# Optimization experiments

Measured on AMD Instinct MI355X. Metric: run time of the kernel, lower is better.

## Reference

```python
import jax, jax.numpy as jnp
import numpy as np

B, N, D = 1, 4096, 512
H, HD = 8, 64
NBINS = 512
CAND = 64
SCALE = 1.0 / np.sqrt(HD)
MAX_NORM = 1.0 - 1e-5
TWO_PI = 2.0 * np.pi


def _project(x):
    # Poincare-ball style projection: clip L2 norm of each point to MAX_NORM.
    n = jnp.sqrt(jnp.sum(x * x, axis=-1, keepdims=True))
    s = jnp.minimum(1.0, MAX_NORM / jnp.maximum(n, 1e-12))
    return x * s


def _bins(x):
    # Deterministic geometric binning (DavisCache stand-in): quantize the
    # angle of the first two coordinates into NBINS bins.
    ang = jnp.arctan2(x[..., 1], x[..., 0])  # (-pi, pi]
    b = jnp.floor((ang / TWO_PI + 0.5) * NBINS)
    return jnp.clip(b, 0, NBINS - 1).astype(jnp.int32)


def setup_inputs() -> dict:
    key0 = jax.random.key(0)
    ks = jax.random.split(key0, 12)
    w = 0.02  # typical init scale for projection weights
    return {
        "query": jax.random.normal(ks[0], (B, N, D), dtype=jnp.float32),
        "key": jax.random.normal(ks[1], (B, N, D), dtype=jnp.float32),
        "value": jax.random.normal(ks[2], (B, N, D), dtype=jnp.float32),
        "Wq": jax.random.normal(ks[3], (D, D), dtype=jnp.float32) * w,
        "bq": jnp.zeros((D,), dtype=jnp.float32),
        "Wk": jax.random.normal(ks[4], (D, D), dtype=jnp.float32) * w,
        "bk": jnp.zeros((D,), dtype=jnp.float32),
        "Wv": jax.random.normal(ks[5], (D, D), dtype=jnp.float32) * w,
        "bv": jnp.zeros((D,), dtype=jnp.float32),
        "Wo": jax.random.normal(ks[6], (D, D), dtype=jnp.float32) * w,
        "bo": jnp.zeros((D,), dtype=jnp.float32),
    }


def reference(query, key, value, Wq, bq, Wk, bk, Wv, bv, Wo, bo):
    Bq, Nq, Dm = query.shape
    Nk = key.shape[1]
    # projections + split heads -> (B, H, N, HD)
    q = (query @ Wq.T + bq).reshape(Bq, Nq, H, HD).transpose(0, 2, 1, 3)
    k = (key @ Wk.T + bk).reshape(Bq, Nk, H, HD).transpose(0, 2, 1, 3)
    v = (value @ Wv.T + bv).reshape(Bq, Nk, H, HD).transpose(0, 2, 1, 3)
    q = _project(q)
    k = _project(k)

    # geometric binning; candidate keys for a query are those whose bin is
    # within radius 1 of the query's bin (neighboring_bins, radius=1).
    qb = _bins(q)  # (B, H, Nq) int32
    kb = _bins(k)  # (B, H, Nk) int32
    mask = jnp.abs(qb[..., :, None] - kb[..., None, :]) <= 1  # (B,H,Nq,Nk)
    # fallback: if a query has no candidates, attend over all keys
    any_valid = jnp.any(mask, axis=-1, keepdims=True)
    eff = jnp.where(any_valid, mask, True)
    # keep only the first CAND candidates per query (by key index)
    rank = jnp.cumsum(eff.astype(jnp.int32), axis=-1) - 1
    sel = eff & (rank < CAND)

    scores = jnp.einsum("bhqd,bhkd->bhqk", q, k) * SCALE
    scores = jnp.where(sel, scores, -jnp.inf)
    attn = jax.nn.softmax(scores, axis=-1)  # dropout p=0.0 (eval mode)
    out = jnp.einsum("bhqk,bhkd->bhqd", attn, v)

    out = out.transpose(0, 2, 1, 3).reshape(Bq, Nq, Dm)
    return out @ Wo.T + bo
```

## Files before the change

kernel.cpp:

```cpp
#include <hip/hip_runtime.h>
#include <math.h>

typedef unsigned short u16;
typedef __attribute__((ext_vector_type(8))) short v8bf;
typedef __attribute__((ext_vector_type(4))) float f32x4;

#define N_TOK 4096
#define DMODEL 512
#define NHEAD 8
#define HDIM 64
#define CANDN 64
#define NBINS 512
#define BINCAP 64
#define QCAP 128
#define ATT_SCALE 0.125f
#define MAX_NORM_F 0.99999f

__device__ __forceinline__ u16 f2bf(float f) {
  union { float f; unsigned int i; } v; v.f = f;
  unsigned int x = v.i;
  return (u16)((x + 0x7fffu + ((x >> 16) & 1u)) >> 16);
}
__device__ __forceinline__ uint4 pack8v(const float4 x0, const float4 x1) {
  union { u16 h[8]; uint4 u; } r;
  r.h[0] = f2bf(x0.x); r.h[1] = f2bf(x0.y); r.h[2] = f2bf(x0.z); r.h[3] = f2bf(x0.w);
  r.h[4] = f2bf(x1.x); r.h[5] = f2bf(x1.y); r.h[6] = f2bf(x1.z); r.h[7] = f2bf(x1.w);
  return r.u;
}

__global__ __launch_bounds__(256) void bins_kernel(
    const float* __restrict__ query, const float* __restrict__ key_,
    const float* __restrict__ Wq, const float* __restrict__ Wk,
    int* __restrict__ qb, int* __restrict__ kb,
    unsigned char* __restrict__ flags, int* __restrict__ khist)
{
  __shared__ float xs[16 * 516];
  const int blk = blockIdx.x;
  const int tid = threadIdx.x;

  if (blk >= 512) {
    int4 z4; z4.x = 0; z4.y = 0; z4.z = 0; z4.w = 0;
#pragma unroll
    for (int i = 0; i < 8; ++i) ((int4*)khist)[tid + i * 256] = z4;
    return;
  }

  const int isk  = blk >> 8;
  const int tile = blk & 255;
  const float* X = isk ? key_ : query;
  const float* W = isk ? Wk : Wq;

#pragma unroll
  for (int i = 0; i < 8; ++i) {
    const int flat = i * 1024 + tid * 4;
    const int row = flat >> 9, col = flat & 511;
    *(float4*)&xs[row * 516 + col] = *(const float4*)(X + (tile * 16 + row) * DMODEL + col);
  }
  __syncthreads();

  const int n_local = tid >> 4;
  const int pair = tid & 15;
  const int h = pair >> 1, coord = pair & 1;
  const float* wrow = W + ((h << 6) + coord) * DMODEL;
  const float* xrow = &xs[n_local * 516];

  double c0 = 0.0, c1 = 0.0, c2 = 0.0, c3 = 0.0;
  for (int k = 0; k < DMODEL; k += 4) {
    const float4 xv = *(const float4*)(xrow + k);
    const float4 wv = *(const float4*)(wrow + k);
    c0 = fma((double)xv.x, (double)wv.x, c0);
    c1 = fma((double)xv.y, (double)wv.y, c1);
    c2 = fma((double)xv.z, (double)wv.z, c2);
    c3 = fma((double)xv.w, (double)wv.w, c3);
  }
  const double a = (c0 + c1) + (c2 + c3);
  const double other = __shfl_xor(a, 1);
  if (coord == 0) {
    const double a0 = a, a1 = other;
    const int n = tile * 16 + n_local;
    double ang = atan2(a1, a0);
    double t = (ang / 6.283185307179586 + 0.5) * 512.0;
    int b = (int)floor(t);
    b = b < 0 ? 0 : (b > 511 ? 511 : b);
    (isk ? kb : qb)[(h << 12) + n] = b;

    const double r = sqrt(a0 * a0 + a1 * a1);
    const double dist = fabs(t - nearbyint(t));
    const double margin = fmin(0.45, 3.3e-4 / fmax(r, 1e-30) + 5e-5);
    flags[(isk << 15) | (h << 12) | n] = (dist < margin) ? 1 : 0;
  }
}

__device__ float fdlibm_atanf(float x) {
#pragma clang fp contract(off)
  const float atanhi[4] = {4.6364760399e-01f, 7.8539812565e-01f,
                           9.8279368877e-01f, 1.5707962513e+00f};
  const float atanlo[4] = {5.0121582440e-09f, 3.7748947079e-08f,
                           3.4473217170e-08f, 7.5497894159e-08f};
  const float aT[5] = {3.3333328366e-01f, -1.9999158382e-01f, 1.4253635705e-01f,
                       -1.0648017377e-01f, 6.1687607318e-02f};
  unsigned ix = __float_as_uint(x);
  const unsigned sign = ix >> 31;
  ix &= 0x7fffffffu;
  int id;
  float z, w, s1, s2;
  if (ix >= 0x4c800000u) {
    z = atanhi[3] + 0x1p-120f;
    return sign ? -z : z;
  }
  if (ix < 0x3ee00000u) {
    if (ix < 0x39800000u) return x;
    id = -1;
  } else {
    x = fabsf(x);
    if (ix < 0x3f980000u) {
      if (ix < 0x3f300000u) { id = 0; x = (2.0f * x - 1.0f) / (2.0f + x); }
      else                  { id = 1; x = (x - 1.0f) / (x + 1.0f); }
    } else {
      if (ix < 0x401c0000u) { id = 2; x = (x - 1.5f) / (1.0f + 1.5f * x); }
      else                  { id = 3; x = -1.0f / x; }
    }
  }
  z = x * x;
  w = z * z;
  s1 = z * (aT[0] + w * (aT[2] + w * aT[4]));
  s2 = w * (aT[1] + w * aT[3]);
  if (id < 0) return x - x * (s1 + s2);
  z = atanhi[id] - ((x * (s1 + s2) - atanlo[id]) - x);
  return sign ? -z : z;
}

__device__ float fdlibm_atan2f(float y, float x) {
#pragma clang fp contract(off)
  const float pi = 3.1415927410e+00f, pi_lo = -8.7422776573e-08f;
  const unsigned hx = __float_as_uint(x), hy = __float_as_uint(y);
  if (hx == 0x3f800000u) return fdlibm_atanf(y);
  const unsigned m = ((hy >> 31) & 1u) | ((hx >> 30) & 2u);
  const unsigned ix = hx & 0x7fffffffu, iy = hy & 0x7fffffffu;
  if (iy == 0u) {
    switch (m) { case 0: case 1: return y; case 2: return pi; default: return -pi; }
  }
  if (ix == 0u) return (m & 1u) ? -1.57079637050628662f : 1.57079637050628662f;
  float z;
  if (ix + (26u << 23) < iy) {
    z = 1.57079637050628662f;
    return (m & 1u) ? -z : z;
  }
  if ((m & 2u) && iy + (26u << 23) < ix) z = 0.0f;
  else z = fdlibm_atanf(fabsf(y / x));
  switch (m) {
    case 0: return z;
    case 1: return -z;
    case 2: return pi - (z - pi_lo);
    default: return (z - pi_lo) - pi;
  }
}

__global__ __launch_bounds__(256) void fixgemm_kernel(
    const float* __restrict__ query, const float* __restrict__ key_,
    const float* __restrict__ value,
    const float* __restrict__ Wq, const float* __restrict__ Wk,
    const float* __restrict__ Wv,
    const float* __restrict__ bq, const float* __restrict__ bk,
    const float* __restrict__ bv,
    const unsigned char* __restrict__ flags,
    int* __restrict__ qb, int* __restrict__ kb,
    u16* __restrict__ Qb, u16* __restrict__ Kb, u16* __restrict__ Vb)
{
  __shared__ __align__(16) char smem[30720];
  __shared__ int wle[64];
  __shared__ int wlc;

  const int blk = blockIdx.x;
  const int tid = threadIdx.x;

  if (blk < 512) {
    const int slice = blk;
    if (tid == 0) wlc = 0;
    __syncthreads();
    if (tid < 128) {
      const int flat = (slice << 7) + tid;
      if (flags[flat]) {
        const int p = atomicAdd(&wlc, 1);
        if (p < 64) wle[p] = flat;
      }
    }
    __syncthreads();
    int nw = wlc; if (nw > 64) nw = 64;
    const int w = tid >> 6, d = tid & 63;
    for (int e = w; e < nw; e += 4) {
      const int flat = wle[e];
      const int n = flat & 4095;
      const int h = (flat >> 12) & 7;
      const int isk = flat >> 15;
      const float* xr = (isk ? key_ : query) + n * DMODEL;
      const float* wr = (isk ? Wk : Wq) + ((h << 6) + d) * DMODEL;
      float acc = 0.0f;
      for (int k = 0; k < DMODEL; k += 16) {
        const float4 xa = *(const float4*)(xr + k);
        const float4 xb = *(const float4*)(xr + k + 4);
        const float4 xc = *(const float4*)(xr + k + 8);
        const float4 xd = *(const float4*)(xr + k + 12);
        const float4 wa = *(const float4*)(wr + k);
        const float4 wb = *(const float4*)(wr + k + 4);
        const float4 wc = *(const float4*)(wr + k + 8);
        const float4 wd = *(const float4*)(wr + k + 12);
        acc = __fmaf_rn(xa.x, wa.x, acc); acc = __fmaf_rn(xa.y, wa.y, acc);
        acc = __fmaf_rn(xa.z, wa.z, acc); acc = __fmaf_rn(xa.w, wa.w, acc);
        acc = __fmaf_rn(xb.x, wb.x, acc); acc = __fmaf_rn(xb.y, wb.y, acc);
        acc = __fmaf_rn(xb.z, wb.z, acc); acc = __fmaf_rn(xb.w, wb.w, acc);
        acc = __fmaf_rn(xc.x, wc.x, acc); acc = __fmaf_rn(xc.y, wc.y, acc);
        acc = __fmaf_rn(xc.z, wc.z, acc); acc = __fmaf_rn(xc.w, wc.w, acc);
        acc = __fmaf_rn(xd.x, wd.x, acc); acc = __fmaf_rn(xd.y, wd.y, acc);
        acc = __fmaf_rn(xd.z, wd.z, acc); acc = __fmaf_rn(xd.w, wd.w, acc);
      }
      {
#pragma clang fp contract(off)
        const float sq = acc * acc;
        float rr[8];
#pragma unroll
        for (int j = 0; j < 8; ++j) rr[j] = __shfl(sq, j);
        for (int i = 8; i < 64; i += 8) {
#pragma unroll
          for (int j = 0; j < 8; ++j) rr[j] += __shfl(sq, i + j);
        }
        const float ss = ((rr[0] + rr[1]) + (rr[2] + rr[3])) +
                         ((rr[4] + rr[5]) + (rr[6] + rr[7]));
        const float nrm = __fsqrt_rn(ss);
        const float s = fminf(1.0f, 0.99999f / fmaxf(nrm, 1e-12f));
        const float c0 = __shfl(acc, 0) * s;
        const float c1 = __shfl(acc, 1) * s;
        const float cr = (float)atan2((double)c1, (double)c0);
        const float fd = fdlibm_atan2f(c1, c0);
        const float tol = fmaxf(fabsf(cr) * 6e-7f, 1e-30f);
        const float ang = (fabsf(fd - cr) <= tol) ? fd : cr;
        const float t = ((ang / 6.2831854820251465f) + 0.5f) * 512.0f;
        int b = (int)floorf(t);
        b = b < 0 ? 0 : (b > 511 ? 511 : b);
        if (d == 0) (isk ? kb : qb)[(h << 12) + n] = b;
      }
    }
    return;
  }

  u16* As = (u16*)smem;
  u16* Ws = (u16*)(smem + 10240);

  const int rel = blk - 512;
  const int z = rel >> 8;
  const int rem = rel & 255;
  const int bm = (rem & 63) * 64;
  const int bn = (rem >> 6) * 128;

  const float* X  = (z == 0) ? query : (z == 1) ? key_ : value;
  const float* WF = (z == 0) ? Wq : (z == 1) ? Wk : Wv;
  const float* bias = (z == 0) ? bq : (z == 1) ? bk : bv;
  u16* O          = (z == 0) ? Qb : (z == 1) ? Kb : Vb;

  const int lane = tid & 63;
  const int wave = tid >> 6;
  const int ra  = tid >> 2;
  const int oa  = (tid & 3) * 8;
  const int wm = (wave & 1) * 32;
  const int wn = (wave >> 1) * 64;
  const int l15 = lane & 15;
  const int quad = lane >> 4;

  f32x4 acc[2][4] = {};

  float4 a0f0 = *(const float4*)(X + (bm + ra) * DMODEL + oa);
  float4 a0f1 = *(const float4*)(X + (bm + ra) * DMODEL + oa + 4);
  float4 w0f0 = *(const float4*)(WF + (bn + ra) * DMODEL + oa);
  float4 w0f1 = *(const float4*)(WF + (bn + ra) * DMODEL + oa + 4);
  float4 w1f0 = *(const float4*)(WF + (bn + ra + 64) * DMODEL + oa);
  float4 w1f1 = *(const float4*)(WF + (bn + ra + 64) * DMODEL + oa + 4);

  for (int kt = 0; kt < DMODEL; kt += 32) {
    const int p = (kt >> 5) & 1;
    *(uint4*)&As[p * 2560 + ra * 40 + oa] = pack8v(a0f0, a0f1);
    *(uint4*)&Ws[p * 5120 + ra * 40 + oa] = pack8v(w0f0, w0f1);
    *(uint4*)&Ws[p * 5120 + (ra + 64) * 40 + oa] = pack8v(w1f0, w1f1);
    __syncthreads();
    if (kt + 32 < DMODEL) {
      a0f0 = *(const float4*)(X + (bm + ra) * DMODEL + kt + 32 + oa);
      a0f1 = *(const float4*)(X + (bm + ra) * DMODEL + kt + 32 + oa + 4);
      w0f0 = *(const float4*)(WF + (bn + ra) * DMODEL + kt + 32 + oa);
      w0f1 = *(const float4*)(WF + (bn + ra) * DMODEL + kt + 32 + oa + 4);
      w1f0 = *(const float4*)(WF + (bn + ra + 64) * DMODEL + kt + 32 + oa);
      w1f1 = *(const float4*)(WF + (bn + ra + 64) * DMODEL + kt + 32 + oa + 4);
    }
    v8bf af[2], bfr[4];
#pragma unroll
    for (int i = 0; i < 2; ++i)
      af[i] = *(const v8bf*)&As[p * 2560 + (wm + i * 16 + l15) * 40 + quad * 8];
#pragma unroll
    for (int j = 0; j < 4; ++j)
      bfr[j] = *(const v8bf*)&Ws[p * 5120 + (wn + j * 16 + l15) * 40 + quad * 8];
#pragma unroll
    for (int i = 0; i < 2; ++i)
#pragma unroll
      for (int j = 0; j < 4; ++j)
        acc[i][j] = __builtin_amdgcn_mfma_f32_16x16x32_bf16(af[i], bfr[j], acc[i][j], 0, 0, 0);
  }

  float bval[4];
#pragma unroll
  for (int j = 0; j < 4; ++j) bval[j] = bias[bn + wn + j * 16 + l15];
  const int h = (bn + wn) >> 6;

#pragma unroll
  for (int i = 0; i < 2; ++i) {
#pragma unroll
    for (int r = 0; r < 4; ++r) {
      const int row = bm + wm + i * 16 + quad * 4 + r;
      float v0 = acc[i][0][r] + bval[0];
      float v1 = acc[i][1][r] + bval[1];
      float v2 = acc[i][2][r] + bval[2];
      float v3 = acc[i][3][r] + bval[3];
      if (z != 2) {
        float ss = v0 * v0 + v1 * v1 + v2 * v2 + v3 * v3;
#pragma unroll
        for (int o = 1; o < 16; o <<= 1) ss += __shfl_xor(ss, o);
        const float s = fminf(1.0f, MAX_NORM_F / fmaxf(sqrtf(ss), 1e-12f));
        v0 *= s; v1 *= s; v2 *= s; v3 *= s;
      }
      const int base = (((h << 12) + row) << 6) + l15;
      O[base +  0] = f2bf(v0); O[base + 16] = f2bf(v1);
      O[base + 32] = f2bf(v2); O[base + 48] = f2bf(v3);
    }
  }
}

__global__ __launch_bounds__(256) void bin_hist_kernel(
    const int* __restrict__ kb, const int* __restrict__ qb,
    int* __restrict__ khist, u16* __restrict__ blist,
    int* __restrict__ qhist, u16* __restrict__ qlist)
{
  const int h = blockIdx.x;
  const int type = blockIdx.y;
  const int* src = type ? qb : kb;
  int* hist = type ? qhist : khist;
  u16* list = type ? qlist : blist;
  const int cap = type ? QCAP : BINCAP;

  const int i = blockIdx.z * 256 + threadIdx.x;
  const int b = src[(h << 12) + i];
  const int pos = atomicAdd(&hist[(h << 9) + b], 1);
  if (pos < cap) list[((h << 9) + b) * cap + pos] = (u16)i;
}

__global__ __launch_bounds__(64) void attn_bin_kernel(
    const u16* __restrict__ Qb, const u16* __restrict__ Kb,
    const u16* __restrict__ Vb, const int* __restrict__ qhist,
    const u16* __restrict__ qlist, const int* __restrict__ khist,
    const u16* __restrict__ blist, u16* __restrict__ aout)
{
  __shared__ u16 kf[4 * 2 * 4 * 16 * 8];
  __shared__ u16 pf[16 * 72];
  __shared__ u16 s_cand[64];
  __shared__ int s_qg[16];

  const int hb = blockIdx.x;
  const int h = hb >> 9;
  const int b = hb & 511;
  int qcnt = qhist[hb];
  if (qcnt > QCAP) qcnt = QCAP;
  if (qcnt == 0) return;

  const int lane = threadIdx.x;
  const int l15 = lane & 15;
  const int quad = lane >> 4;

  int v0 = 0xFFFF, v1 = 0xFFFF, v2 = 0xFFFF;
  int c0 = 0, c1 = 0, c2 = 0;
  if (b > 0) {
    c0 = khist[(h << 9) + b - 1];
    if (c0 > BINCAP) c0 = BINCAP;
    if (lane < c0) v0 = (int)blist[(((h << 9) + b - 1) << 6) + lane];
  }
  {
    c1 = khist[(h << 9) + b];
    if (c1 > BINCAP) c1 = BINCAP;
    if (lane < c1) v1 = (int)blist[(((h << 9) + b) << 6) + lane];
  }
  if (b < NBINS - 1) {
    c2 = khist[(h << 9) + b + 1];
    if (c2 > BINCAP) c2 = BINCAP;
    if (lane < c2) v2 = (int)blist[(((h << 9) + b + 1) << 6) + lane];
  }

  int r0 = 0, r1 = 0, r2 = 0;
#pragma unroll 8
  for (int j = 0; j < 64; ++j) {
    const int w0 = __shfl(v0, j);
    const int w1 = __shfl(v1, j);
    const int w2 = __shfl(v2, j);
    r0 += (w0 < v0) + (w1 < v0) + (w2 < v0);
    r1 += (w0 < v1) + (w1 < v1) + (w2 < v1);
    r2 += (w0 < v2) + (w1 < v2) + (w2 < v2);
  }
  const int tot = c0 + c1 + c2;
  const int ccnt = tot < CANDN ? tot : CANDN;
  const int ccnt_eff = (tot == 0) ? 64 : ccnt;
  if (tot == 0) {
    s_cand[lane] = (u16)lane;
  } else {
    if (v0 != 0xFFFF && r0 < CANDN) s_cand[r0] = (u16)v0;
    if (v1 != 0xFFFF && r1 < CANDN) s_cand[r1] = (u16)v1;
    if (v2 != 0xFFFF && r2 < CANDN) s_cand[r2] = (u16)v2;
  }
  __syncthreads();
  if (tot > 0 && lane >= ccnt) s_cand[lane] = s_cand[0];
  __syncthreads();

  {
    const int r = lane >> 3, s = lane & 7;
    const int ks = s >> 2, qd = s & 3;
#pragma unroll
    for (int it = 0; it < 8; ++it) {
      const int key = it * 8 + r;
      const int c = s_cand[key];
      const uint4 kv = *(const uint4*)(Kb + ((h << 18) | (c << 6)) + s * 8);
      const int idx = ((((key >> 4) * 2 + ks) * 4 + qd) * 16 + (key & 15)) * 8;
      *(uint4*)&kf[idx] = kv;
    }
  }
  __syncthreads();
  v8bf akf[4][2];
#pragma unroll
  for (int t = 0; t < 4; ++t)
#pragma unroll
    for (int ks = 0; ks < 2; ++ks)
      akf[t][ks] = *(const v8bf*)&kf[(((t * 2 + ks) * 4 + quad) * 16 + l15) * 8];
  __syncthreads();

  {
    const int r = lane >> 3, s = lane & 7;
    const int nt = s >> 1, d0 = (s & 1) * 8;
#pragma unroll
    for (int it = 0; it < 8; ++it) {
      const int key = it * 8 + r;
      const int c = s_cand[key];
      union { u16 hh[8]; uint4 u; } vv;
      vv.u = *(const uint4*)(Vb + ((h << 18) | (c << 6)) + s * 8);
      const int kstep = key >> 5, qd = (key >> 3) & 3, j = key & 7;
#pragma unroll
      for (int m = 0; m < 8; ++m)
        kf[(((nt * 2 + kstep) * 4 + qd) * 16 + d0 + m) * 8 + j] = vv.hh[m];
    }
  }
  __syncthreads();
  v8bf bvf[4][2];
#pragma unroll
  for (int t = 0; t < 4; ++t)
#pragma unroll
    for (int ks = 0; ks < 2; ++ks)
      bvf[t][ks] = *(const v8bf*)&kf[(((t * 2 + ks) * 4 + quad) * 16 + l15) * 8];

  const int nchunk = (qcnt + 15) >> 4;
  for (int ci = 0; ci < nchunk; ++ci) {
    const int base = ci << 4;
    const int qcn = min(16, qcnt - base);
    __syncthreads();
    if (lane < 16) {
      int idx = base + lane;
      if (idx > qcnt - 1) idx = qcnt - 1;
      s_qg[lane] = (int)qlist[(hb << 7) + idx];
    }
    __syncthreads();

    const u16* qrow = Qb + ((h << 18) | (s_qg[l15] << 6));
    v8bf bq[2];
#pragma unroll
    for (int ks = 0; ks < 2; ++ks)
      bq[ks] = *(const v8bf*)(qrow + ks * 32 + quad * 8);

    float sc[16];
    __builtin_amdgcn_s_setprio(1);
#pragma unroll
    for (int t = 0; t < 4; ++t) {
      f32x4 sa = {0.f, 0.f, 0.f, 0.f};
      sa = __builtin_amdgcn_mfma_f32_16x16x32_bf16(akf[t][0], bq[0], sa, 0, 0, 0);
      sa = __builtin_amdgcn_mfma_f32_16x16x32_bf16(akf[t][1], bq[1], sa, 0, 0, 0);
#pragma unroll
      for (int r = 0; r < 4; ++r) {
        const int key = t * 16 + quad * 4 + r;
        sc[t * 4 + r] = (key < ccnt_eff) ? sa[r] * ATT_SCALE : -INFINITY;
      }
    }
    __builtin_amdgcn_s_setprio(0);
    float mx = sc[0];
#pragma unroll
    for (int i = 1; i < 16; ++i) mx = fmaxf(mx, sc[i]);
    mx = fmaxf(mx, __shfl_xor(mx, 16));
    mx = fmaxf(mx, __shfl_xor(mx, 32));
    float sum = 0.0f;
    float pe[16];
#pragma unroll
    for (int i = 0; i < 16; ++i) { pe[i] = __expf(sc[i] - mx); sum += pe[i]; }
    sum += __shfl_xor(sum, 16);
    sum += __shfl_xor(sum, 32);
    const float inv = 1.0f / sum;

    __syncthreads();
#pragma unroll
    for (int t = 0; t < 4; ++t)
#pragma unroll
      for (int r = 0; r < 4; ++r)
        pf[l15 * 72 + t * 16 + quad * 4 + r] = f2bf(pe[t * 4 + r] * inv);
    __syncthreads();

    v8bf ap[2];
#pragma unroll
    for (int ks = 0; ks < 2; ++ks)
      ap[ks] = *(const v8bf*)&pf[l15 * 72 + ks * 32 + quad * 8];

    __builtin_amdgcn_s_setprio(1);
#pragma unroll
    for (int nt = 0; nt < 4; ++nt) {
      f32x4 o = {0.f, 0.f, 0.f, 0.f};
      o = __builtin_amdgcn_mfma_f32_16x16x32_bf16(ap[0], bvf[nt][0], o, 0, 0, 0);
      o = __builtin_amdgcn_mfma_f32_16x16x32_bf16(ap[1], bvf[nt][1], o, 0, 0, 0);
#pragma unroll
      for (int r = 0; r < 4; ++r) {
        const int row = quad * 4 + r;
        if (row < qcn)
          aout[s_qg[row] * DMODEL + (h << 6) + nt * 16 + l15] = f2bf(o[r]);
      }
    }
    __builtin_amdgcn_s_setprio(0);
  }
}

__global__ __launch_bounds__(256) void gemm_out_kernel(
    const u16* __restrict__ A, const float* __restrict__ WF,
    const float* __restrict__ bias, float* __restrict__ O)
{
  __shared__ u16 As[2][64 * 40];
  __shared__ u16 Ws[2][64 * 40];

  const int tid  = threadIdx.x;
  const int lane = tid & 63;
  const int wave = tid >> 6;
  const int ra  = tid >> 2;
  const int oa  = (tid & 3) * 8;

  const int bm = blockIdx.x * 64;
  const int bn = blockIdx.y * 64;
  const int wm = (wave & 1) * 32;
  const int wn = (wave >> 1) * 32;
  const int l15 = lane & 15;
  const int quad = lane >> 4;

  f32x4 acc[2][2] = {};

  uint4 a0 = *(const uint4*)(A + (bm + ra) * DMODEL + oa);
  float4 w0f0 = *(const float4*)(WF + (bn + ra) * DMODEL + oa);
  float4 w0f1 = *(const float4*)(WF + (bn + ra) * DMODEL + oa + 4);

  for (int kt = 0; kt < DMODEL; kt += 32) {
    const int p = (kt >> 5) & 1;
    *(uint4*)&As[p][ra * 40 + oa] = a0;
    *(uint4*)&Ws[p][ra * 40 + oa] = pack8v(w0f0, w0f1);
    __syncthreads();
    if (kt + 32 < DMODEL) {
      a0 = *(const uint4*)(A + (bm + ra) * DMODEL + kt + 32 + oa);
      w0f0 = *(const float4*)(WF + (bn + ra) * DMODEL + kt + 32 + oa);
      w0f1 = *(const float4*)(WF + (bn + ra) * DMODEL + kt + 32 + oa + 4);
    }
    v8bf af[2], bfr[2];
#pragma unroll
    for (int i = 0; i < 2; ++i)
      af[i] = *(const v8bf*)&As[p][(wm + i * 16 + l15) * 40 + quad * 8];
#pragma unroll
    for (int j = 0; j < 2; ++j)
      bfr[j] = *(const v8bf*)&Ws[p][(wn + j * 16 + l15) * 40 + quad * 8];
#pragma unroll
    for (int i = 0; i < 2; ++i)
#pragma unroll
      for (int j = 0; j < 2; ++j)
        acc[i][j] = __builtin_amdgcn_mfma_f32_16x16x32_bf16(af[i], bfr[j], acc[i][j], 0, 0, 0);
  }

#pragma unroll
  for (int j = 0; j < 2; ++j) {
    const int cg = bn + wn + j * 16 + l15;
    const float bval = bias[cg];
#pragma unroll
    for (int i = 0; i < 2; ++i) {
      const int rbase = bm + wm + i * 16 + quad * 4;
#pragma unroll
      for (int r = 0; r < 4; ++r)
        O[(rbase + r) * DMODEL + cg] = acc[i][j][r] + bval;
    }
  }
}

extern "C" void kernel_launch(void* const* d_in, const int* in_sizes, int n_in,
                              void* d_out, int out_size, void* d_ws, size_t ws_size,
                              hipStream_t stream) {
  const float* query = (const float*)d_in[0];
  const float* key_  = (const float*)d_in[1];
  const float* value = (const float*)d_in[2];
  const float* Wq = (const float*)d_in[3];
  const float* bq = (const float*)d_in[4];
  const float* Wk = (const float*)d_in[5];
  const float* bk = (const float*)d_in[6];
  const float* Wv = (const float*)d_in[7];
  const float* bv = (const float*)d_in[8];
  const float* Wo = (const float*)d_in[9];
  const float* bo = (const float*)d_in[10];

  char* ws = (char*)d_ws;
  u16* Qb    = (u16*)(ws + 14680064);
  u16* Kb    = (u16*)(ws + 18874368);
  u16* Vb    = (u16*)(ws + 23068672);
  u16* aout  = (u16*)(ws + 27262976);
  int* qb    = (int*)(ws + 31457280);
  int* kb    = (int*)(ws + 31588352);
  unsigned char* flags = (unsigned char*)(ws + 31719424);
  int* khist = (int*)(ws + 31784960);
  int* qhist = (int*)(ws + 31801344);
  u16* blist = (u16*)(ws + 31817728);
  u16* qlist = (u16*)(ws + 32342016);

  bins_kernel<<<513, 256, 0, stream>>>(
      query, key_, Wq, Wk, qb, kb, flags, khist);
  fixgemm_kernel<<<1280, 256, 0, stream>>>(
      query, key_, value, Wq, Wk, Wv, bq, bk, bv,
      flags, qb, kb, Qb, Kb, Vb);
  bin_hist_kernel<<<dim3(8, 2, 16), 256, 0, stream>>>(
      kb, qb, khist, blist, qhist, qlist);
  attn_bin_kernel<<<4096, 64, 0, stream>>>(
      Qb, Kb, Vb, qhist, qlist, khist, blist, aout);
  gemm_out_kernel<<<dim3(64, 8), 256, 0, stream>>>(aout, Wo, bo, (float*)d_out);
}
```

Before: 194.9 us.

## Fuse bin fix-up into bins kernel and histogram into projection GEMM

After: 194.8 us. Within noise of the previous version (-0.1%).

```diff
diff --git a/kernel.cpp b/kernel.cpp
--- a/kernel.cpp
+++ b/kernel.cpp
@@ -26,69 +26,6 @@
   r.h[0] = f2bf(x0.x); r.h[1] = f2bf(x0.y); r.h[2] = f2bf(x0.z); r.h[3] = f2bf(x0.w);
   r.h[4] = f2bf(x1.x); r.h[5] = f2bf(x1.y); r.h[6] = f2bf(x1.z); r.h[7] = f2bf(x1.w);
   return r.u;
-}
-
-__global__ __launch_bounds__(256) void bins_kernel(
-    const float* __restrict__ query, const float* __restrict__ key_,
-    const float* __restrict__ Wq, const float* __restrict__ Wk,
-    int* __restrict__ qb, int* __restrict__ kb,
-    unsigned char* __restrict__ flags, int* __restrict__ khist)
-{
-  __shared__ float xs[16 * 516];
-  const int blk = blockIdx.x;
-  const int tid = threadIdx.x;
-
-  if (blk >= 512) {
-    int4 z4; z4.x = 0; z4.y = 0; z4.z = 0; z4.w = 0;
-#pragma unroll
-    for (int i = 0; i < 8; ++i) ((int4*)khist)[tid + i * 256] = z4;
-    return;
-  }
-
-  const int isk  = blk >> 8;
-  const int tile = blk & 255;
-  const float* X = isk ? key_ : query;
-  const float* W = isk ? Wk : Wq;
-
-#pragma unroll
-  for (int i = 0; i < 8; ++i) {
-    const int flat = i * 1024 + tid * 4;
-    const int row = flat >> 9, col = flat & 511;
-    *(float4*)&xs[row * 516 + col] = *(const float4*)(X + (tile * 16 + row) * DMODEL + col);
-  }
-  __syncthreads();
-
-  const int n_local = tid >> 4;
-  const int pair = tid & 15;
-  const int h = pair >> 1, coord = pair & 1;
-  const float* wrow = W + ((h << 6) + coord) * DMODEL;
-  const float* xrow = &xs[n_local * 516];
-
-  double c0 = 0.0, c1 = 0.0, c2 = 0.0, c3 = 0.0;
-  for (int k = 0; k < DMODEL; k += 4) {
-    const float4 xv = *(const float4*)(xrow + k);
-    const float4 wv = *(const float4*)(wrow + k);
-    c0 = fma((double)xv.x, (double)wv.x, c0);
-    c1 = fma((double)xv.y, (double)wv.y, c1);
-    c2 = fma((double)xv.z, (double)wv.z, c2);
-    c3 = fma((double)xv.w, (double)wv.w, c3);
-  }
-  const double a = (c0 + c1) + (c2 + c3);
-  const double other = __shfl_xor(a, 1);
-  if (coord == 0) {
-    const double a0 = a, a1 = other;
-    const int n = tile * 16 + n_local;
-    double ang = atan2(a1, a0);
-    double t = (ang / 6.283185307179586 + 0.5) * 512.0;
-    int b = (int)floor(t);
-    b = b < 0 ? 0 : (b > 511 ? 511 : b);
-    (isk ? kb : qb)[(h << 12) + n] = b;
-
-    const double r = sqrt(a0 * a0 + a1 * a1);
-    const double dist = fabs(t - nearbyint(t));
-    const double margin = fmin(0.45, 3.3e-4 / fmax(r, 1e-30) + 5e-5);
-    flags[(isk << 15) | (h << 12) | n] = (dist < margin) ? 1 : 0;
-  }
 }
 
 __device__ float fdlibm_atanf(float x) {
@@ -156,99 +93,170 @@
   }
 }
 
-__global__ __launch_bounds__(256) void fixgemm_kernel(
+__global__ __launch_bounds__(256) void binsfix_kernel(
+    const float* __restrict__ query, const float* __restrict__ key_,
+    const float* __restrict__ Wq, const float* __restrict__ Wk,
+    int* __restrict__ qb, int* __restrict__ kb, int* __restrict__ khist)
+{
+  __shared__ float xs[16 * 516];
+  __shared__ int wle[64];
+  __shared__ int wlc;
+  const int blk = blockIdx.x;
+  const int tid = threadIdx.x;
+
+  if (blk >= 512) {
+    int4 z4; z4.x = 0; z4.y = 0; z4.z = 0; z4.w = 0;
+#pragma unroll
+    for (int i = 0; i < 8; ++i) ((int4*)khist)[tid + i * 256] = z4;
+    return;
+  }
+
+  const int isk  = blk >> 8;
+  const int tile = blk & 255;
+  const float* X = isk ? key_ : query;
+  const float* W = isk ? Wk : Wq;
+
+#pragma unroll
+  for (int i = 0; i < 8; ++i) {
+    const int flat = i * 1024 + tid * 4;
+    const int row = flat >> 9, col = flat & 511;
+    *(float4*)&xs[row * 516 + col] = *(const float4*)(X + (tile * 16 + row) * DMODEL + col);
+  }
+  if (tid == 0) wlc = 0;
+  __syncthreads();
+
+  {
+    const int n_local = tid >> 4;
+    const int pair = tid & 15;
+    const int h = pair >> 1, coord = pair & 1;
+    const float* wrow = W + ((h << 6) + coord) * DMODEL;
+    const float* xrow = &xs[n_local * 516];
+
+    double c0 = 0.0, c1 = 0.0, c2 = 0.0, c3 = 0.0;
+    for (int k = 0; k < DMODEL; k += 4) {
+      const float4 xv = *(const float4*)(xrow + k);
+      const float4 wv = *(const float4*)(wrow + k);
+      c0 = fma((double)xv.x, (double)wv.x, c0);
+      c1 = fma((double)xv.y, (double)wv.y, c1);
+      c2 = fma((double)xv.z, (double)wv.z, c2);
+      c3 = fma((double)xv.w, (double)wv.w, c3);
+    }
+    const double a = (c0 + c1) + (c2 + c3);
+    const double other = __shfl_xor(a, 1);
+    if (coord == 0) {
+      const double a0 = a, a1 = other;
+      const int n = tile * 16 + n_local;
+      double ang = atan2(a1, a0);
+      double t = (ang / 6.283185307179586 + 0.5) * 512.0;
+      int b = (int)floor(t);
+      b = b < 0 ? 0 : (b > 511 ? 511 : b);
+
+      const double r = sqrt(a0 * a0 + a1 * a1);
+      const double dist = fabs(t - nearbyint(t));
+      const double margin = fmin(0.45, 3.3e-4 / fmax(r, 1e-30) + 5e-5);
+      if (dist < margin) {
+        const int p = atomicAdd(&wlc, 1);
+        if (p < 64) wle[p] = (h << 4) | n_local;
+        else (isk ? kb : qb)[(h << 12) + n] = b;
+      } else {
+        (isk ? kb : qb)[(h << 12) + n] = b;
+      }
+    }
+  }
+  __syncthreads();
+
+  int nw = wlc; if (nw > 64) nw = 64;
+  const int w = tid >> 6, d = tid & 63;
+  for (int e = w; e < nw; e += 4) {
+    const int n_local2 = wle[e] & 15;
+    const int h2 = wle[e] >> 4;
+    const int n = tile * 16 + n_local2;
+    const float* xr = &xs[n_local2 * 516];
+    const float* wr = W + ((h2 << 6) + d) * DMODEL;
+    float acc = 0.0f;
+    for (int k = 0; k < DMODEL; k += 16) {
+      const float4 xa = *(const float4*)(xr + k);
+      const float4 xb = *(const float4*)(xr + k + 4);
+      const float4 xc = *(const float4*)(xr + k + 8);
+      const float4 xd = *(const float4*)(xr + k + 12);
+      const float4 wa = *(const float4*)(wr + k);
+      const float4 wb = *(const float4*)(wr + k + 4);
+      const float4 wc = *(const float4*)(wr + k + 8);
+      const float4 wd = *(const float4*)(wr + k + 12);
+      acc = __fmaf_rn(xa.x, wa.x, acc); acc = __fmaf_rn(xa.y, wa.y, acc);
+      acc = __fmaf_rn(xa.z, wa.z, acc); acc = __fmaf_rn(xa.w, wa.w, acc);
+      acc = __fmaf_rn(xb.x, wb.x, acc); acc = __fmaf_rn(xb.y, wb.y, acc);
+      acc = __fmaf_rn(xb.z, wb.z, acc); acc = __fmaf_rn(xb.w, wb.w, acc);
+      acc = __fmaf_rn(xc.x, wc.x, acc); acc = __fmaf_rn(xc.y, wc.y, acc);
+      acc = __fmaf_rn(xc.z, wc.z, acc); acc = __fmaf_rn(xc.w, wc.w, acc);
+      acc = __fmaf_rn(xd.x, wd.x, acc); acc = __fmaf_rn(xd.y, wd.y, acc);
+      acc = __fmaf_rn(xd.z, wd.z, acc); acc = __fmaf_rn(xd.w, wd.w, acc);
+    }
+    {
+#pragma clang fp contract(off)
+      const float sq = acc * acc;
+      float rr[8];
+#pragma unroll
+      for (int j = 0; j < 8; ++j) rr[j] = __shfl(sq, j);
+      for (int i = 8; i < 64; i += 8) {
+#pragma unroll
+        for (int j = 0; j < 8; ++j) rr[j] += __shfl(sq, i + j);
+      }
+      const float ss = ((rr[0] + rr[1]) + (rr[2] + rr[3])) +
+                       ((rr[4] + rr[5]) + (rr[6] + rr[7]));
+      const float nrm = __fsqrt_rn(ss);
+      const float s = fminf(1.0f, 0.99999f / fmaxf(nrm, 1e-12f));
+      const float c0 = __shfl(acc, 0) * s;
+      const float c1 = __shfl(acc, 1) * s;
+      const float cr = (float)atan2((double)c1, (double)c0);
+      const float fd = fdlibm_atan2f(c1, c0);
+      const float tol = fmaxf(fabsf(cr) * 6e-7f, 1e-30f);
+      const float ang = (fabsf(fd - cr) <= tol) ? fd : cr;
+      const float t = ((ang / 6.2831854820251465f) + 0.5f) * 512.0f;
+      int b = (int)floorf(t);
+      b = b < 0 ? 0 : (b > 511 ? 511 : b);
+      if (d == 0) (isk ? kb : qb)[(h2 << 12) + n] = b;
+    }
+  }
+}
+
+__global__ __launch_bounds__(256) void gemmhist_kernel(
     const float* __restrict__ query, const float* __restrict__ key_,
     const float* __restrict__ value,
     const float* __restrict__ Wq, const float* __restrict__ Wk,
     const float* __restrict__ Wv,
     const float* __restrict__ bq, const float* __restrict__ bk,
     const float* __restrict__ bv,
-    const unsigned char* __restrict__ flags,
-    int* __restrict__ qb, int* __restrict__ kb,
+    const int* __restrict__ qb, const int* __restrict__ kb,
+    int* __restrict__ khist, u16* __restrict__ blist,
+    int* __restrict__ qhist, u16* __restrict__ qlist,
     u16* __restrict__ Qb, u16* __restrict__ Kb, u16* __restrict__ Vb)
 {
   __shared__ __align__(16) char smem[30720];
-  __shared__ int wle[64];
-  __shared__ int wlc;
-
   const int blk = blockIdx.x;
   const int tid = threadIdx.x;
 
-  if (blk < 512) {
-    const int slice = blk;
-    if (tid == 0) wlc = 0;
-    __syncthreads();
-    if (tid < 128) {
-      const int flat = (slice << 7) + tid;
-      if (flags[flat]) {
-        const int p = atomicAdd(&wlc, 1);
-        if (p < 64) wle[p] = flat;
-      }
-    }
-    __syncthreads();
-    int nw = wlc; if (nw > 64) nw = 64;
-    const int w = tid >> 6, d = tid & 63;
-    for (int e = w; e < nw; e += 4) {
-      const int flat = wle[e];
-      const int n = flat & 4095;
-      const int h = (flat >> 12) & 7;
-      const int isk = flat >> 15;
-      const float* xr = (isk ? key_ : query) + n * DMODEL;
-      const float* wr = (isk ? Wk : Wq) + ((h << 6) + d) * DMODEL;
-      float acc = 0.0f;
-      for (int k = 0; k < DMODEL; k += 16) {
-        const float4 xa = *(const float4*)(xr + k);
-        const float4 xb = *(const float4*)(xr + k + 4);
-        const float4 xc = *(const float4*)(xr + k + 8);
-        const float4 xd = *(const float4*)(xr + k + 12);
-        const float4 wa = *(const float4*)(wr + k);
-        const float4 wb = *(const float4*)(wr + k + 4);
-        const float4 wc = *(const float4*)(wr + k + 8);
-        const float4 wd = *(const float4*)(wr + k + 12);
-        acc = __fmaf_rn(xa.x, wa.x, acc); acc = __fmaf_rn(xa.y, wa.y, acc);
-        acc = __fmaf_rn(xa.z, wa.z, acc); acc = __fmaf_rn(xa.w, wa.w, acc);
-        acc = __fmaf_rn(xb.x, wb.x, acc); acc = __fmaf_rn(xb.y, wb.y, acc);
-        acc = __fmaf_rn(xb.z, wb.z, acc); acc = __fmaf_rn(xb.w, wb.w, acc);
-        acc = __fmaf_rn(xc.x, wc.x, acc); acc = __fmaf_rn(xc.y, wc.y, acc);
-        acc = __fmaf_rn(xc.z, wc.z, acc); acc = __fmaf_rn(xc.w, wc.w, acc);
-        acc = __fmaf_rn(xd.x, wd.x, acc); acc = __fmaf_rn(xd.y, wd.y, acc);
-        acc = __fmaf_rn(xd.z, wd.z, acc); acc = __fmaf_rn(xd.w, wd.w, acc);
-      }
-      {
-#pragma clang fp contract(off)
-        const float sq = acc * acc;
-        float rr[8];
-#pragma unroll
-        for (int j = 0; j < 8; ++j) rr[j] = __shfl(sq, j);
-        for (int i = 8; i < 64; i += 8) {
-#pragma unroll
-          for (int j = 0; j < 8; ++j) rr[j] += __shfl(sq, i + j);
-        }
-        const float ss = ((rr[0] + rr[1]) + (rr[2] + rr[3])) +
-                         ((rr[4] + rr[5]) + (rr[6] + rr[7]));
-        const float nrm = __fsqrt_rn(ss);
-        const float s = fminf(1.0f, 0.99999f / fmaxf(nrm, 1e-12f));
-        const float c0 = __shfl(acc, 0) * s;
-        const float c1 = __shfl(acc, 1) * s;
-        const float cr = (float)atan2((double)c1, (double)c0);
-        const float fd = fdlibm_atan2f(c1, c0);
-        const float tol = fmaxf(fabsf(cr) * 6e-7f, 1e-30f);
-        const float ang = (fabsf(fd - cr) <= tol) ? fd : cr;
-        const float t = ((ang / 6.2831854820251465f) + 0.5f) * 512.0f;
-        int b = (int)floorf(t);
-        b = b < 0 ? 0 : (b > 511 ? 511 : b);
-        if (d == 0) (isk ? kb : qb)[(h << 12) + n] = b;
-      }
-    }
+  if (blk >= 768) {
+    const int rel = blk - 768;
+    const int h = rel & 7;
+    const int type = (rel >> 3) & 1;
+    const int chunk = rel >> 4;
+    const int* src = type ? qb : kb;
+    int* hist = type ? qhist : khist;
+    u16* list = type ? qlist : blist;
+    const int cap = type ? QCAP : BINCAP;
+    const int i = (chunk << 8) + tid;
+    const int b = src[(h << 12) + i];
+    const int pos = atomicAdd(&hist[(h << 9) + b], 1);
+    if (pos < cap) list[((h << 9) + b) * cap + pos] = (u16)i;
     return;
   }
 
   u16* As = (u16*)smem;
   u16* Ws = (u16*)(smem + 10240);
 
-  const int rel = blk - 512;
-  const int z = rel >> 8;
-  const int rem = rel & 255;
+  const int z = blk >> 8;
+  const int rem = blk & 255;
   const int bm = (rem & 63) * 64;
   const int bn = (rem >> 6) * 128;
 
@@ -329,24 +337,6 @@
       O[base + 32] = f2bf(v2); O[base + 48] = f2bf(v3);
     }
   }
-}
-
-__global__ __launch_bounds__(256) void bin_hist_kernel(
-    const int* __restrict__ kb, const int* __restrict__ qb,
-    int* __restrict__ khist, u16* __restrict__ blist,
-    int* __restrict__ qhist, u16* __restrict__ qlist)
-{
-  const int h = blockIdx.x;
-  const int type = blockIdx.y;
-  const int* src = type ? qb : kb;
-  int* hist = type ? qhist : khist;
-  u16* list = type ? qlist : blist;
-  const int cap = type ? QCAP : BINCAP;
-
-  const int i = blockIdx.z * 256 + threadIdx.x;
-  const int b = src[(h << 12) + i];
-  const int pos = atomicAdd(&hist[(h << 9) + b], 1);
-  if (pos < cap) list[((h << 9) + b) * cap + pos] = (u16)i;
 }
 
 __global__ __launch_bounds__(64) void attn_bin_kernel(
@@ -618,19 +608,16 @@
   u16* aout  = (u16*)(ws + 27262976);
   int* qb    = (int*)(ws + 31457280);
   int* kb    = (int*)(ws + 31588352);
-  unsigned char* flags = (unsigned char*)(ws + 31719424);
   int* khist = (int*)(ws + 31784960);
   int* qhist = (int*)(ws + 31801344);
   u16* blist = (u16*)(ws + 31817728);
   u16* qlist = (u16*)(ws + 32342016);
 
-  bins_kernel<<<513, 256, 0, stream>>>(
-      query, key_, Wq, Wk, qb, kb, flags, khist);
-  fixgemm_kernel<<<1280, 256, 0, stream>>>(
+  binsfix_kernel<<<513, 256, 0, stream>>>(
+      query, key_, Wq, Wk, qb, kb, khist);
+  gemmhist_kernel<<<1024, 256, 0, stream>>>(
       query, key_, value, Wq, Wk, Wv, bq, bk, bv,
-      flags, qb, kb, Qb, Kb, Vb);
-  bin_hist_kernel<<<dim3(8, 2, 16), 256, 0, stream>>>(
-      kb, qb, khist, blist, qhist, qlist);
+      qb, kb, khist, blist, qhist, qlist, Qb, Kb, Vb);
   attn_bin_kernel<<<4096, 64, 0, stream>>>(
       Qb, Kb, Vb, qhist, qlist, khist, blist, aout);
   gemm_out_kernel<<<dim3(64, 8), 256, 0, stream>>>(aout, Wo, bo, (float*)d_out);
```
